# Kernel optimization log

Measured on AMD Instinct MI355X. Metric: run time of the kernel, lower is better.

The kernel has to match this reference:

```python
import jax, jax.numpy as jnp
import numpy as np

N_NODES = 4096
DEG_HALF = 16
MAX_E = 64
D = 128
H = 4
L = 2
N_SPECIES = 4
R_CUT = 5.0
R_TRANS = 3.0


def _layer_norm(x, w, b, eps=1e-5):
    m = jnp.mean(x, axis=-1, keepdims=True)
    v = jnp.mean((x - m) ** 2, axis=-1, keepdims=True)
    return (x - m) * jax.lax.rsqrt(v + eps) * w + b


def _transformer(x, radial_mask, p):
    # x: (N, MAX_E, D); radial_mask: (N, MAX_E). Pre-LN transformer whose
    # attention weights are reweighted by the radial cutoff mask over keys.
    ln1_w, ln1_b, qkv_w, qkv_b, out_w, out_b, ln2_w, ln2_b, m1_w, m1_b, m2_w, m2_b = p
    n, s, d = x.shape
    dh = d // H
    scale = np.float32(1.0 / np.sqrt(dh))
    for l in range(L):
        h = _layer_norm(x, ln1_w[l], ln1_b[l])
        qkv = h @ qkv_w[l] + qkv_b[l]  # (n, s, 3d)
        q, k, v = jnp.split(qkv, 3, axis=-1)
        q = q.reshape(n, s, H, dh).transpose(0, 2, 1, 3)
        k = k.reshape(n, s, H, dh).transpose(0, 2, 1, 3)
        v = v.reshape(n, s, H, dh).transpose(0, 2, 1, 3)
        a = jax.nn.softmax(jnp.einsum("nhqc,nhkc->nhqk", q, k) * scale, axis=-1)
        a = a * radial_mask[:, None, None, :]
        a = a / (jnp.sum(a, axis=-1, keepdims=True) + 1e-9)
        o = jnp.einsum("nhqk,nhkc->nhqc", a, v).transpose(0, 2, 1, 3).reshape(n, s, d)
        x = x + o @ out_w[l] + out_b[l]
        h = _layer_norm(x, ln2_w[l], ln2_b[l])
        x = x + jax.nn.gelu(h @ m1_w[l] + m1_b[l]) @ m2_w[l] + m2_b[l]
    return x


def _forward(edge_vectors, enc_cart_w, enc_center_emb, enc_neighbor_emb, enc_comp_w,
             t0, t1, gnn_w, last_w, comp_w,
             species_index, centers, neighbors, nef_indices, nef_mask,
             nef_to_edges_neighbor, corresponding_edges):
    r = jnp.sqrt(jnp.sum(edge_vectors ** 2, axis=-1))
    radial = jnp.where(r < R_TRANS, 1.0,
                       0.5 * (jnp.cos(jnp.pi * (r - R_TRANS) / (R_CUT - R_TRANS)) + 1.0))
    radial = jnp.where(r < R_CUT, radial, 0.0)
    eic = species_index[centers]
    ein = species_index[neighbors]
    # edge_array_to_nef gathers
    ev_nef = edge_vectors[nef_indices]                  # (N, MAX_E, 3)
    rm = jnp.where(nef_mask, radial[nef_indices], 0.0)  # (N, MAX_E)
    enc = jnp.concatenate([ev_nef @ enc_cart_w,
                           enc_center_emb[eic[nef_indices]],
                           enc_neighbor_emb[ein[nef_indices]]], axis=-1)
    feat = enc @ enc_comp_w                             # (N, MAX_E, D)
    feat = _transformer(feat, rm, t0)
    # one message-passing round (num_gnn_layers=2 -> 1 MP layer)
    edge_feat = feat[centers, nef_to_edges_neighbor]    # NEF -> edge list, (E, D)
    new = jnp.concatenate([edge_feat, edge_feat[corresponding_edges]], axis=-1) @ gnn_w
    new = _transformer(new[nef_indices], rm, t1)        # edge list -> NEF
    feat = feat + new
    node_features = jnp.sum(feat * rm[..., None], axis=1)  # masked scatter-sum
    return node_features @ last_w + comp_w[species_index][:, None]  # (N, 1)


def setup_inputs() -> dict:
    rng = np.random.default_rng(0)
    src = np.repeat(np.arange(N_NODES), DEG_HALF)
    dst = (src + rng.integers(1, N_NODES, size=src.shape[0])) % N_NODES
    centers = np.concatenate([src, dst]).astype(np.int64)
    neighbors = np.concatenate([dst, src]).astype(np.int64)
    E = centers.shape[0]
    corresponding_edges = np.concatenate([np.arange(E // 2, E), np.arange(E // 2)]).astype(np.int64)
    order = np.argsort(centers, kind="stable")
    sc = centers[order]
    starts = np.searchsorted(sc, np.arange(N_NODES))
    ranks = np.arange(E) - starts[sc]
    assert ranks.max() < MAX_E
    nef_indices = np.zeros((N_NODES, MAX_E), np.int64)
    nef_mask = np.zeros((N_NODES, MAX_E), bool)
    nef_indices[sc, ranks] = order
    nef_mask[sc, ranks] = True
    nef_to_edges_neighbor = np.zeros(E, np.int64)
    nef_to_edges_neighbor[order] = ranks
    half = rng.standard_normal((E // 2, 3)) * 1.6
    edge_vectors = np.concatenate([half, -half]).astype(np.float32)
    species_index = rng.integers(0, N_SPECIES, N_NODES).astype(np.int64)

    keys = iter(jax.random.split(jax.random.key(0), 80))

    def lin(shape, fan_in):
        return jax.random.normal(next(keys), shape, jnp.float32) / np.float32(np.sqrt(fan_in))

    inp = {
        "edge_vectors": jnp.asarray(edge_vectors),
        "enc_cart_w": lin((3, D), 3),
        "enc_center_emb": lin((N_SPECIES, D), 1),
        "enc_neighbor_emb": lin((N_SPECIES, D), 1),
        "enc_comp_w": lin((3 * D, D), 3 * D),
        "gnn_w": lin((2 * D, D), 2 * D),
        "last_w": lin((D, 1), D),
        "comp_w": lin((N_SPECIES,), 1),
        "species_index": jnp.asarray(species_index),
        "centers": jnp.asarray(centers),
        "neighbors": jnp.asarray(neighbors),
        "nef_indices": jnp.asarray(nef_indices),
        "nef_mask": jnp.asarray(nef_mask),
        "nef_to_edges_neighbor": jnp.asarray(nef_to_edges_neighbor),
        "corresponding_edges": jnp.asarray(corresponding_edges),
    }
    for t in ("t0", "t1"):
        inp[t + "_ln1_w"] = jnp.ones((L, D), jnp.float32)
        inp[t + "_ln1_b"] = jnp.zeros((L, D), jnp.float32)
        inp[t + "_qkv_w"] = lin((L, D, 3 * D), D)
        inp[t + "_qkv_b"] = jnp.zeros((L, 3 * D), jnp.float32)
        inp[t + "_out_w"] = lin((L, D, D), D)
        inp[t + "_out_b"] = jnp.zeros((L, D), jnp.float32)
        inp[t + "_ln2_w"] = jnp.ones((L, D), jnp.float32)
        inp[t + "_ln2_b"] = jnp.zeros((L, D), jnp.float32)
        inp[t + "_mlp1_w"] = lin((L, D, 4 * D), D)
        inp[t + "_mlp1_b"] = jnp.zeros((L, 4 * D), jnp.float32)
        inp[t + "_mlp2_w"] = lin((L, 4 * D, D), 4 * D)
        inp[t + "_mlp2_b"] = jnp.zeros((L, D), jnp.float32)
    return inp


def reference(edge_vectors, enc_cart_w, enc_center_emb, enc_neighbor_emb, enc_comp_w,
              t0_ln1_w, t0_ln1_b, t0_qkv_w, t0_qkv_b, t0_out_w, t0_out_b,
              t0_ln2_w, t0_ln2_b, t0_mlp1_w, t0_mlp1_b, t0_mlp2_w, t0_mlp2_b,
              t1_ln1_w, t1_ln1_b, t1_qkv_w, t1_qkv_b, t1_out_w, t1_out_b,
              t1_ln2_w, t1_ln2_b, t1_mlp1_w, t1_mlp1_b, t1_mlp2_w, t1_mlp2_b,
              gnn_w, last_w, comp_w,
              species_index, centers, neighbors, nef_indices, nef_mask,
              nef_to_edges_neighbor, corresponding_edges):
    t0 = (t0_ln1_w, t0_ln1_b, t0_qkv_w, t0_qkv_b, t0_out_w, t0_out_b,
          t0_ln2_w, t0_ln2_b, t0_mlp1_w, t0_mlp1_b, t0_mlp2_w, t0_mlp2_b)
    t1 = (t1_ln1_w, t1_ln1_b, t1_qkv_w, t1_qkv_b, t1_out_w, t1_out_b,
          t1_ln2_w, t1_ln2_b, t1_mlp1_w, t1_mlp1_b, t1_mlp2_w, t1_mlp2_b)
    return _forward(edge_vectors, enc_cart_w, enc_center_emb, enc_neighbor_emb, enc_comp_w,
                    t0, t1, gnn_w, last_w, comp_w,
                    species_index, centers, neighbors, nef_indices, nef_mask,
                    nef_to_edges_neighbor, corresponding_edges)
```

## Files before the change

### kernel.cpp

```cpp
#include <hip/hip_runtime.h>

typedef short s8v __attribute__((ext_vector_type(8)));
typedef float f4v __attribute__((ext_vector_type(4)));

#define MFMA16(a,b,c) __builtin_amdgcn_mfma_f32_16x16x32_bf16((a),(b),(c),0,0,0)

#define N_NODES 4096
#define N_EDGE  131072
#define ATT_SCALE 0.17677669529663687f
#define NGC2     -1.5957691216057308f

__device__ __forceinline__ unsigned short f2bf(float f) {
  union { float f; unsigned u; } v; v.f = f;
  return (unsigned short)((v.u + 0x8000u) >> 16);
}
__device__ __forceinline__ unsigned short f2bf_rne(float f) {
  union { float f; unsigned u; } v; v.f = f;
  unsigned r = v.u + 0x7fffu + ((v.u >> 16) & 1u);
  return (unsigned short)(r >> 16);
}
__device__ __forceinline__ float bf2f(short s) {
  union { unsigned u; float f; } v;
  v.u = ((unsigned)(unsigned short)s) << 16;
  return v.f;
}
__device__ __forceinline__ int iclamp(int v, int lo, int hi) {
  return v < lo ? lo : (v > hi ? hi : v);
}


__global__ void k_tr(const float* __restrict__ src, short* __restrict__ dst,
                     int L, int K, int N) {
  int idx = blockIdx.x * 256 + threadIdx.x;
  int tot = L * K * N;
  if (idx >= tot) return;
  int l = idx / (K * N);
  int r = idx - l * (K * N);
  int k = r / N;
  int n = r - k * N;
  dst[l * K * N + n * K + k] = (short)f2bf_rne(src[idx]);
}

__global__ void k_tabs(const float* __restrict__ cart, const float* __restrict__ cemb,
                       const float* __restrict__ nemb, const float* __restrict__ comp,
                       float* __restrict__ tabs) {
  int idx = blockIdx.x * 256 + threadIdx.x;
  if (idx >= 1408) return;
  float s = 0.f;
  if (idx < 384) {
    int i = idx >> 7, d = idx & 127;
    for (int j = 0; j < 128; ++j) s += cart[i * 128 + j] * comp[j * 128 + d];
  } else if (idx < 896) {
    int i2 = idx - 384; int sp = i2 >> 7, d = i2 & 127;
    for (int j = 0; j < 128; ++j) s += cemb[sp * 128 + j] * comp[(128 + j) * 128 + d];
  } else {
    int i2 = idx - 896; int sp = i2 >> 7, d = i2 & 127;
    for (int j = 0; j < 128; ++j) s += nemb[sp * 128 + j] * comp[(256 + j) * 128 + d];
  }
  tabs[idx] = s;
}

__global__ void k_rm(const float* __restrict__ ev, const int* __restrict__ centers,
                     const int* __restrict__ nef2, float* __restrict__ rm) {
  int e = blockIdx.x * 256 + threadIdx.x;
  if (e >= N_EDGE) return;
  float x = ev[e*3], y = ev[e*3+1], z = ev[e*3+2];
  float r = sqrtf(x*x + y*y + z*z);
  float rad;
  if (r < 3.0f)      rad = 1.0f;
  else if (r < 5.0f) rad = 0.5f * (cosf(3.14159265358979f * (r - 3.0f) * 0.5f) + 1.0f);
  else               rad = 0.0f;
  int c  = iclamp(centers[e], 0, N_NODES - 1);
  int rk = iclamp(nef2[e], 0, 63);
  rm[c * 64 + rk] = rad;
}

__global__ __launch_bounds__(256) void k_enc(
    const float* __restrict__ ev, const int* __restrict__ nef,
    const int* __restrict__ centers, const int* __restrict__ neighbors,
    const int* __restrict__ species, const float* __restrict__ tabs,
    short* __restrict__ feat) {
  int n = blockIdx.x, t = threadIdx.x, j = t >> 2, qq = t & 3;
  int e = iclamp(nef[n * 64 + j], 0, N_EDGE - 1);
  float e0 = ev[e*3], e1 = ev[e*3+1], e2 = ev[e*3+2];
  int nc = iclamp(centers[e],   0, N_NODES - 1);
  int nn = iclamp(neighbors[e], 0, N_NODES - 1);
  int sc = iclamp(species[nc], 0, 3), sn = iclamp(species[nn], 0, 3);
  const float* m0 = tabs + qq*32;
  const float* m1 = tabs + 128 + qq*32;
  const float* m2 = tabs + 256 + qq*32;
  const float* tc = tabs + 384 + sc*128 + qq*32;
  const float* tn = tabs + 896 + sn*128 + qq*32;
  short* o = feat + ((size_t)(n*64 + j))*128 + qq*32;
  #pragma unroll
  for (int i = 0; i < 32; i += 2) {
    float a = e0*m0[i]   + e1*m1[i]   + e2*m2[i]   + tc[i]   + tn[i];
    float b = e0*m0[i+1] + e1*m1[i+1] + e2*m2[i+1] + tc[i+1] + tn[i+1];
    *(unsigned*)(o + i) = (unsigned)f2bf_rne(a) | ((unsigned)f2bf_rne(b) << 16);
  }
}


__device__ __forceinline__ void ln_sub(float (&xr)[4][2][4],
                                       const float* __restrict__ gw, const float* __restrict__ gb,
                                       float* red, short* hb, int wid, int quad, int l4) {
  #pragma unroll
  for (int mt = 0; mt < 4; ++mt)
    #pragma unroll
    for (int reg = 0; reg < 4; ++reg) {
      float a = xr[mt][0][reg] + xr[mt][1][reg];
      float s = xr[mt][0][reg]*xr[mt][0][reg] + xr[mt][1][reg]*xr[mt][1][reg];
      #pragma unroll
      for (int m = 1; m < 16; m <<= 1) { a += __shfl_xor(a, m); s += __shfl_xor(s, m); }
      if (l4 == 0) {
        int r = mt*16 + quad*4 + reg;
        red[(wid*64 + r)*2]     = a;
        red[(wid*64 + r)*2 + 1] = s;
      }
    }
  __syncthreads();
  int tid = threadIdx.x;
  if (tid < 64) {
    float a = 0.f, s = 0.f;
    #pragma unroll
    for (int w = 0; w < 4; ++w) { a += red[(w*64 + tid)*2]; s += red[(w*64 + tid)*2 + 1]; }
    float mean = a * (1.f/128.f);
    float var  = s * (1.f/128.f) - mean*mean;
    red[tid*2]     = mean;
    red[tid*2 + 1] = rsqrtf(var + 1e-5f);
  }
  __syncthreads();
  float gv[2], bv[2];
  #pragma unroll
  for (int nt = 0; nt < 2; ++nt) { int c = wid*32 + nt*16 + l4; gv[nt] = gw[c]; bv[nt] = gb[c]; }
  #pragma unroll
  for (int mt = 0; mt < 4; ++mt)
    #pragma unroll
    for (int reg = 0; reg < 4; ++reg) {
      int r = mt*16 + quad*4 + reg;
      float mean = red[r*2], inv = red[r*2 + 1];
      #pragma unroll
      for (int nt = 0; nt < 2; ++nt) {
        float h = (xr[mt][nt][reg] - mean) * inv * gv[nt] + bv[nt];
        hb[r*136 + wid*32 + nt*16 + l4] = (short)f2bf(h);
      }
    }
  __syncthreads();
}

__global__ __launch_bounds__(256, 2) void k_tf(
    short* __restrict__ x, const float* __restrict__ rm,
    const float* __restrict__ lnw1, const float* __restrict__ lnb1,
    const short* __restrict__ qkvT, const float* __restrict__ qkvb,
    const short* __restrict__ outT, const float* __restrict__ outb,
    const float* __restrict__ lnw2, const float* __restrict__ lnb2,
    const short* __restrict__ m1T, const float* __restrict__ m1b,
    const short* __restrict__ m2T, const float* __restrict__ m2b) {
  __shared__ __align__(16) char smem[53248];
  short* hb  = (short*)smem;
  short* kb  = (short*)(smem + 17408);
  short* vtb = (short*)(smem + 34816);
  float* red = (float*)(smem + 34816);

  const int tid = threadIdx.x;
  const int wid = tid >> 6;
  const int lane = tid & 63;
  const int l4 = lane & 15;
  const int quad = lane >> 4;
  const int n = blockIdx.x;

  short* xg = x + (size_t)n * 64 * 128;
  float xr[4][2][4];
  #pragma unroll
  for (int mt = 0; mt < 4; ++mt)
    #pragma unroll
    for (int nt = 0; nt < 2; ++nt)
      #pragma unroll
      for (int reg = 0; reg < 4; ++reg)
        xr[mt][nt][reg] = bf2f(xg[(mt*16 + quad*4 + reg)*128 + wid*32 + nt*16 + l4]);

  for (int l = 0; l < 2; ++l) {
    const float* g1    = lnw1 + l*128;   const float* bb1   = lnb1 + l*128;
    const short* qkvTl = qkvT + l*49152; const float* qkvbl = qkvb + l*384;
    const short* outTl = outT + l*16384; const float* outbl = outb + l*128;
    const float* g2    = lnw2 + l*128;   const float* bb2   = lnb2 + l*128;
    const short* m1Tl  = m1T + l*65536;  const float* m1bl  = m1b + l*512;
    const short* m2Tl  = m2T + l*65536;  const float* m2bl  = m2b + l*128;

    __syncthreads();

    ln_sub(xr, g1, bb1, red, hb, wid, quad, l4);

    #pragma unroll 1
    for (int hh = 0; hh < 2; ++hh) {
      s8v af[2][4];
      #pragma unroll
      for (int m2 = 0; m2 < 2; ++m2)
        #pragma unroll
        for (int k0 = 0; k0 < 4; ++k0)
          af[m2][k0] = *(const s8v*)(hb + ((hh*2 + m2)*16 + l4)*136 + k0*32 + quad*8);
      __syncthreads();

      #pragma unroll 1
      for (int j = 0; j < 6; ++j) {
        int col = wid*96 + j*16 + l4;
        s8v bf[4];
        #pragma unroll
        for (int k0 = 0; k0 < 4; ++k0)
          bf[k0] = *(const s8v*)(qkvTl + col*128 + k0*32 + quad*8);
        float bias = qkvbl[col];
        f4v acc[2];
        #pragma unroll
        for (int m2 = 0; m2 < 2; ++m2) { f4v bb = {bias,bias,bias,bias}; acc[m2] = bb; }
        #pragma unroll
        for (int k0 = 0; k0 < 4; ++k0)
          #pragma unroll
          for (int m2 = 0; m2 < 2; ++m2)
            acc[m2] = MFMA16(af[m2][k0], bf[k0], acc[m2]);
        if (col < 128) {
          #pragma unroll
          for (int m2 = 0; m2 < 2; ++m2)
            #pragma unroll
            for (int reg = 0; reg < 4; ++reg)
              hb[((hh*2+m2)*16 + quad*4 + reg)*136 + col] = (short)f2bf(acc[m2][reg] * ATT_SCALE);
        } else if (col < 256) {
          int c = col - 128;
          #pragma unroll
          for (int m2 = 0; m2 < 2; ++m2)
            #pragma unroll
            for (int reg = 0; reg < 4; ++reg)
              kb[((hh*2+m2)*16 + quad*4 + reg)*136 + c] = (short)f2bf(acc[m2][reg]);
        } else {
          int c = col - 256;
          #pragma unroll
          for (int m2 = 0; m2 < 2; ++m2)
            #pragma unroll
            for (int reg = 0; reg < 4; ++reg)
              vtb[c*72 + (hh*2+m2)*16 + quad*4 + reg] = (short)f2bf(acc[m2][reg]);
        }
      }
    }
    __syncthreads();

    {
      const int h = wid;
      float rv[4];
      #pragma unroll
      for (int n2 = 0; n2 < 4; ++n2) rv[n2] = rm[n*64 + n2*16 + l4];

      #pragma unroll 1
      for (int hh = 0; hh < 2; ++hh) {
        #pragma unroll 1
        for (int m2 = 0; m2 < 2; ++m2) {
          const int row0 = (hh*2 + m2)*16;
          f4v S[4];
          {
            s8v aq = *(const s8v*)(hb + (row0 + l4)*136 + h*32 + quad*8);
            s8v bk0 = *(const s8v*)(kb + (      l4)*136 + h*32 + quad*8);
            s8v bk1 = *(const s8v*)(kb + (16 + l4)*136 + h*32 + quad*8);
            s8v bk2 = *(const s8v*)(kb + (32 + l4)*136 + h*32 + quad*8);
            s8v bk3 = *(const s8v*)(kb + (48 + l4)*136 + h*32 + quad*8);
            f4v zz = {0.f,0.f,0.f,0.f};
            S[0] = MFMA16(aq, bk0, zz);
            S[1] = MFMA16(aq, bk1, zz);
            S[2] = MFMA16(aq, bk2, zz);
            S[3] = MFMA16(aq, bk3, zz);
          }

          #pragma unroll
          for (int reg = 0; reg < 4; ++reg) {
            float mx = fmaxf(fmaxf(S[0][reg], S[1][reg]),
                             fmaxf(S[2][reg], S[3][reg]));
            mx = fmaxf(mx, __shfl_xor(mx, 1));
            mx = fmaxf(mx, __shfl_xor(mx, 2));
            mx = fmaxf(mx, __shfl_xor(mx, 4));
            mx = fmaxf(mx, __shfl_xor(mx, 8));
            float E = 0.f, W = 0.f;
            #pragma unroll
            for (int n2 = 0; n2 < 4; ++n2) {
              float e = __expf(S[n2][reg] - mx);
              E += e; W += e * rv[n2];
              S[n2][reg] = e * rv[n2];
            }
            E += __shfl_xor(E, 1); E += __shfl_xor(E, 2);
            E += __shfl_xor(E, 4); E += __shfl_xor(E, 8);
            W += __shfl_xor(W, 1); W += __shfl_xor(W, 2);
            W += __shfl_xor(W, 4); W += __shfl_xor(W, 8);
            float inv = __builtin_amdgcn_rcpf(W + 1e-9f * E);
            #pragma unroll
            for (int n2 = 0; n2 < 4; ++n2) S[n2][reg] *= inv;
          }

          f4v o[2];
          { f4v zz = {0.f,0.f,0.f,0.f}; o[0] = zz; o[1] = zz; }
          #pragma unroll
          for (int c = 0; c < 2; ++c) {
            #pragma unroll
            for (int n2 = 0; n2 < 2; ++n2)
              #pragma unroll
              for (int reg = 0; reg < 4; ++reg)
                hb[(row0 + quad*4 + reg)*136 + h*32 + n2*16 + l4] =
                    (short)f2bf(S[2*c + n2][reg]);
            s8v ap = *(const s8v*)(hb + (row0 + l4)*136 + h*32 + quad*8);
            #pragma unroll
            for (int nt = 0; nt < 2; ++nt) {
              s8v bv = *(const s8v*)(vtb + (h*32 + nt*16 + l4)*72 + c*32 + quad*8);
              o[nt] = MFMA16(ap, bv, o[nt]);
            }
          }
          #pragma unroll
          for (int nt = 0; nt < 2; ++nt)
            #pragma unroll
            for (int reg = 0; reg < 4; ++reg)
              hb[(row0 + quad*4 + reg)*136 + h*32 + nt*16 + l4] =
                  (short)f2bf(o[nt][reg]);
        }
      }
    }
    __syncthreads();

    #pragma unroll
    for (int hh = 0; hh < 2; ++hh) {
      s8v ao[2][4];
      #pragma unroll
      for (int m2 = 0; m2 < 2; ++m2)
        #pragma unroll
        for (int k0 = 0; k0 < 4; ++k0)
          ao[m2][k0] = *(const s8v*)(hb + ((hh*2+m2)*16 + l4)*136 + k0*32 + quad*8);
      #pragma unroll
      for (int nt = 0; nt < 2; ++nt) {
        int c = wid*32 + nt*16 + l4;
        s8v bo[4];
        #pragma unroll
        for (int k0 = 0; k0 < 4; ++k0)
          bo[k0] = *(const s8v*)(outTl + c*128 + k0*32 + quad*8);
        float bias = outbl[c];
        #pragma unroll
        for (int m2 = 0; m2 < 2; ++m2) {
          int mt = hh*2 + m2;
          f4v a2 = {xr[mt][nt][0] + bias, xr[mt][nt][1] + bias,
                    xr[mt][nt][2] + bias, xr[mt][nt][3] + bias};
          #pragma unroll
          for (int k0 = 0; k0 < 4; ++k0)
            a2 = MFMA16(ao[m2][k0], bo[k0], a2);
          #pragma unroll
          for (int reg = 0; reg < 4; ++reg)
            xr[mt][nt][reg] = a2[reg];
        }
      }
    }

    ln_sub(xr, g2, bb2, red, hb, wid, quad, l4);

    #pragma unroll 1
    for (int cc = 0; cc < 4; ++cc) {
      short* G = (cc & 1) ? vtb : kb;
      #pragma unroll 1
      for (int hh = 0; hh < 2; ++hh) {
        s8v afm[2][4];
        #pragma unroll
        for (int m2 = 0; m2 < 2; ++m2)
          #pragma unroll
          for (int k0 = 0; k0 < 4; ++k0)
            afm[m2][k0] = *(const s8v*)(hb + ((hh*2+m2)*16 + l4)*136 + k0*32 + quad*8);
        #pragma unroll
        for (int nt = 0; nt < 2; ++nt) {
          int jc = cc*128 + wid*32 + nt*16 + l4;
          s8v bm[4];
          #pragma unroll
          for (int k0 = 0; k0 < 4; ++k0)
            bm[k0] = *(const s8v*)(m1Tl + jc*128 + k0*32 + quad*8);
          float bias = m1bl[jc];
          #pragma unroll
          for (int m2 = 0; m2 < 2; ++m2) {
            f4v a2 = {bias, bias, bias, bias};
            #pragma unroll
            for (int k0 = 0; k0 < 4; ++k0)
              a2 = MFMA16(afm[m2][k0], bm[k0], a2);
            #pragma unroll
            for (int reg = 0; reg < 4; ++reg) {
              float v = a2[reg];
              float t = v * v;
              float u = fmaf(0.044715f, t, 1.0f);
              float w = v * u;
              float e = __expf(NGC2 * w);
              float gl = v * __builtin_amdgcn_rcpf(e + 1.0f);
              G[((hh*2+m2)*16 + quad*4 + reg)*136 + wid*32 + nt*16 + l4] = (short)f2bf(gl);
            }
          }
        }
      }
      __syncthreads();
      #pragma unroll
      for (int hh = 0; hh < 2; ++hh) {
        s8v at4[2][4];
        #pragma unroll
        for (int m2 = 0; m2 < 2; ++m2)
          #pragma unroll
          for (int k0 = 0; k0 < 4; ++k0)
            at4[m2][k0] = *(const s8v*)(G + ((hh*2+m2)*16 + l4)*136 + k0*32 + quad*8);
        #pragma unroll
        for (int nt = 0; nt < 2; ++nt) {
          int c = wid*32 + nt*16 + l4;
          s8v b2f[4];
          #pragma unroll
          for (int k0 = 0; k0 < 4; ++k0)
            b2f[k0] = *(const s8v*)(m2Tl + c*512 + cc*128 + k0*32 + quad*8);
          #pragma unroll
          for (int m2 = 0; m2 < 2; ++m2) {
            int mt = hh*2 + m2;
            f4v a2 = {xr[mt][nt][0], xr[mt][nt][1], xr[mt][nt][2], xr[mt][nt][3]};
            #pragma unroll
            for (int k0 = 0; k0 < 4; ++k0)
              a2 = MFMA16(at4[m2][k0], b2f[k0], a2);
            #pragma unroll
            for (int reg = 0; reg < 4; ++reg)
              xr[mt][nt][reg] = a2[reg];
          }
        }
      }
    }
    #pragma unroll
    for (int nt = 0; nt < 2; ++nt) {
      float b = m2bl[wid*32 + nt*16 + l4];
      #pragma unroll
      for (int mt = 0; mt < 4; ++mt)
        #pragma unroll
        for (int reg = 0; reg < 4; ++reg)
          xr[mt][nt][reg] += b;
    }
  }

  #pragma unroll
  for (int mt = 0; mt < 4; ++mt)
    #pragma unroll
    for (int nt = 0; nt < 2; ++nt)
      #pragma unroll
      for (int reg = 0; reg < 4; ++reg)
        xg[(mt*16 + quad*4 + reg)*128 + wid*32 + nt*16 + l4] = (short)f2bf(xr[mt][nt][reg]);
}

__global__ __launch_bounds__(256) void k_gnn(
    const short* __restrict__ feat, const int* __restrict__ nef,
    const int* __restrict__ corr, const int* __restrict__ centers,
    const int* __restrict__ nef2, const short* __restrict__ gnnT,
    short* __restrict__ out) {
  __shared__ __align__(16) short Ab[64 * 264];
  int n = blockIdx.x, t = threadIdx.x;
  int wid = t >> 6, lane = t & 63, l4 = lane & 15, quad = lane >> 4;
  int j = t >> 2, qq = t & 3;
  int e  = iclamp(nef[n*64 + j], 0, N_EDGE - 1);
  int ce = iclamp(corr[e], 0, N_EDGE - 1);
  size_t r1 = ((size_t)iclamp(centers[e],  0, N_NODES-1) * 64 + iclamp(nef2[e],  0, 63)) * 128;
  size_t r2 = ((size_t)iclamp(centers[ce], 0, N_NODES-1) * 64 + iclamp(nef2[ce], 0, 63)) * 128;
  {
    const s8v* p1 = (const s8v*)(feat + r1 + qq*32);
    const s8v* p2 = (const s8v*)(feat + r2 + qq*32);
    #pragma unroll
    for (int ii = 0; ii < 4; ++ii) {
      *(s8v*)(Ab + j*264 + qq*32 + ii*8)       = p1[ii];
      *(s8v*)(Ab + j*264 + 128 + qq*32 + ii*8) = p2[ii];
    }
  }
  __syncthreads();
  f4v acc[4][2];
  #pragma unroll
  for (int mt = 0; mt < 4; ++mt)
    #pragma unroll
    for (int nt = 0; nt < 2; ++nt) { f4v zz = {0.f,0.f,0.f,0.f}; acc[mt][nt] = zz; }
  #pragma unroll
  for (int k0 = 0; k0 < 8; ++k0) {
    s8v a[4];
    #pragma unroll
    for (int mt = 0; mt < 4; ++mt)
      a[mt] = *(const s8v*)(Ab + (mt*16 + l4)*264 + k0*32 + quad*8);
    #pragma unroll
    for (int nt = 0; nt < 2; ++nt) {
      s8v b = *(const s8v*)(gnnT + (wid*32 + nt*16 + l4)*256 + k0*32 + quad*8);
      #pragma unroll
      for (int mt = 0; mt < 4; ++mt)
        acc[mt][nt] = MFMA16(a[mt], b, acc[mt][nt]);
    }
  }
  #pragma unroll
  for (int mt = 0; mt < 4; ++mt)
    #pragma unroll
    for (int nt = 0; nt < 2; ++nt)
      #pragma unroll
      for (int reg = 0; reg < 4; ++reg)
        out[((size_t)n*64 + mt*16 + quad*4 + reg)*128 + wid*32 + nt*16 + l4] =
            (short)f2bf(acc[mt][nt][reg]);
}

__global__ __launch_bounds__(256) void k_final(
    const short* __restrict__ feat, const short* __restrict__ buf2,
    const float* __restrict__ rm, const float* __restrict__ lastw,
    const float* __restrict__ compw, const int* __restrict__ species,
    float* __restrict__ out) {
  __shared__ float part[4];
  int n = blockIdx.x, t = threadIdx.x;
  int wid = t >> 6, lane = t & 63;
  int j = t >> 2, qq = t & 3;
  size_t base = ((size_t)n*64 + j)*128 + qq*32;
  float s = 0.f;
  #pragma unroll
  for (int i = 0; i < 32; ++i)
    s += (bf2f(feat[base + i]) + bf2f(buf2[base + i])) * lastw[qq*32 + i];
  s += __shfl_xor(s, 1);
  s += __shfl_xor(s, 2);
  float v = (qq == 0) ? s * rm[n*64 + j] : 0.f;
  v += __shfl_xor(v, 4);  v += __shfl_xor(v, 8);
  v += __shfl_xor(v, 16); v += __shfl_xor(v, 32);
  if (lane == 0) part[wid] = v;
  __syncthreads();
  if (t == 0) out[n] = part[0] + part[1] + part[2] + part[3]
                       + compw[iclamp(species[n], 0, 3)];
}


extern "C" void kernel_launch(void* const* d_in, const int* in_sizes, int n_in,
                              void* d_out, int out_size, void* d_ws, size_t ws_size,
                              hipStream_t stream) {
  const float* ev      = (const float*)d_in[0];
  const float* cart    = (const float*)d_in[1];
  const float* cemb    = (const float*)d_in[2];
  const float* nemb    = (const float*)d_in[3];
  const float* comp    = (const float*)d_in[4];
  const float* gnnw    = (const float*)d_in[5];
  const float* lastw   = (const float*)d_in[6];
  const float* compw   = (const float*)d_in[7];
  const int*   species = (const int*)d_in[8];
  const int*   centers = (const int*)d_in[9];
  const int*   neighbors = (const int*)d_in[10];
  const int*   nef     = (const int*)d_in[11];
  const int*   nef2    = (const int*)d_in[13];
  const int*   corr    = (const int*)d_in[14];

  const size_t OFF_RM   = 0;
  const size_t OFF_FEAT = 1048576;
  const size_t OFF_BUF2 = 68157440;
  const size_t OFF_TABS = 135266304;
  const size_t OFF_WBF  = 135271936;
  const size_t NEED     = 136910336;
  if (ws_size < NEED) return;

  char* ws = (char*)d_ws;
  float* rm   = (float*)(ws + OFF_RM);
  short* feat = (short*)(ws + OFF_FEAT);
  short* buf2 = (short*)(ws + OFF_BUF2);
  float* tabs = (float*)(ws + OFF_TABS);
  short* wbf  = (short*)(ws + OFF_WBF);

  short* t0q  = wbf + 0;
  short* t0o  = wbf + 98304;
  short* t0m1 = wbf + 131072;
  short* t0m2 = wbf + 262144;
  short* t1q  = wbf + 393216;
  short* t1o  = wbf + 491520;
  short* t1m1 = wbf + 524288;
  short* t1m2 = wbf + 655360;
  short* gnnT = wbf + 786432;

  hipMemsetAsync(rm, 0, 4096*64*sizeof(float), stream);

  k_tr<<<384, 256, 0, stream>>>((const float*)d_in[17], t0q,  2, 128, 384);
  k_tr<<<128, 256, 0, stream>>>((const float*)d_in[19], t0o,  2, 128, 128);
  k_tr<<<512, 256, 0, stream>>>((const float*)d_in[23], t0m1, 2, 128, 512);
  k_tr<<<512, 256, 0, stream>>>((const float*)d_in[25], t0m2, 2, 512, 128);
  k_tr<<<384, 256, 0, stream>>>((const float*)d_in[29], t1q,  2, 128, 384);
  k_tr<<<128, 256, 0, stream>>>((const float*)d_in[31], t1o,  2, 128, 128);
  k_tr<<<512, 256, 0, stream>>>((const float*)d_in[35], t1m1, 2, 128, 512);
  k_tr<<<512, 256, 0, stream>>>((const float*)d_in[37], t1m2, 2, 512, 128);
  k_tr<<<128, 256, 0, stream>>>(gnnw, gnnT, 1, 256, 128);
  k_tabs<<<6, 256, 0, stream>>>(cart, cemb, nemb, comp, tabs);
  k_rm<<<512, 256, 0, stream>>>(ev, centers, nef2, rm);
  k_enc<<<4096, 256, 0, stream>>>(ev, nef, centers, neighbors, species, tabs, feat);

  k_tf<<<4096, 256, 0, stream>>>(feat, rm,
      (const float*)d_in[15], (const float*)d_in[16], t0q, (const float*)d_in[18],
      t0o, (const float*)d_in[20], (const float*)d_in[21], (const float*)d_in[22],
      t0m1, (const float*)d_in[24], t0m2, (const float*)d_in[26]);

  k_gnn<<<4096, 256, 0, stream>>>(feat, nef, corr, centers, nef2, gnnT, buf2);

  k_tf<<<4096, 256, 0, stream>>>(buf2, rm,
      (const float*)d_in[27], (const float*)d_in[28], t1q, (const float*)d_in[30],
      t1o, (const float*)d_in[32], (const float*)d_in[33], (const float*)d_in[34],
      t1m1, (const float*)d_in[36], t1m2, (const float*)d_in[38]);

  k_final<<<4096, 256, 0, stream>>>(feat, buf2, rm, lastw, compw, species, (float*)d_out);
}
```

Baseline: 1.654 ms.

## Split transformer block work across eight waves per node instead of four

```diff
diff --git a/kernel.cpp b/kernel.cpp
--- a/kernel.cpp
+++ b/kernel.cpp
@@ -101,15 +101,15 @@
 }
 
 
-__device__ __forceinline__ void ln_sub(float (&xr)[4][2][4],
-                                       const float* __restrict__ gw, const float* __restrict__ gb,
-                                       float* red, short* hb, int wid, int quad, int l4) {
+__device__ __forceinline__ void ln_sub8(float (&xr)[4][4],
+                                        const float* __restrict__ gw, const float* __restrict__ gb,
+                                        float* red, short* hb, int wid, int quad, int l4, int tid) {
   #pragma unroll
   for (int mt = 0; mt < 4; ++mt)
     #pragma unroll
     for (int reg = 0; reg < 4; ++reg) {
-      float a = xr[mt][0][reg] + xr[mt][1][reg];
-      float s = xr[mt][0][reg]*xr[mt][0][reg] + xr[mt][1][reg]*xr[mt][1][reg];
+      float a = xr[mt][reg];
+      float s = a * a;
       #pragma unroll
       for (int m = 1; m < 16; m <<= 1) { a += __shfl_xor(a, m); s += __shfl_xor(s, m); }
       if (l4 == 0) {
@@ -119,36 +119,31 @@
       }
     }
   __syncthreads();
-  int tid = threadIdx.x;
   if (tid < 64) {
     float a = 0.f, s = 0.f;
     #pragma unroll
-    for (int w = 0; w < 4; ++w) { a += red[(w*64 + tid)*2]; s += red[(w*64 + tid)*2 + 1]; }
+    for (int w = 0; w < 8; ++w) { a += red[(w*64 + tid)*2]; s += red[(w*64 + tid)*2 + 1]; }
     float mean = a * (1.f/128.f);
     float var  = s * (1.f/128.f) - mean*mean;
     red[tid*2]     = mean;
     red[tid*2 + 1] = rsqrtf(var + 1e-5f);
   }
   __syncthreads();
-  float gv[2], bv[2];
-  #pragma unroll
-  for (int nt = 0; nt < 2; ++nt) { int c = wid*32 + nt*16 + l4; gv[nt] = gw[c]; bv[nt] = gb[c]; }
+  int cw = wid*16 + l4;
+  float gv = gw[cw], bvv = gb[cw];
   #pragma unroll
   for (int mt = 0; mt < 4; ++mt)
     #pragma unroll
     for (int reg = 0; reg < 4; ++reg) {
       int r = mt*16 + quad*4 + reg;
       float mean = red[r*2], inv = red[r*2 + 1];
-      #pragma unroll
-      for (int nt = 0; nt < 2; ++nt) {
-        float h = (xr[mt][nt][reg] - mean) * inv * gv[nt] + bv[nt];
-        hb[r*136 + wid*32 + nt*16 + l4] = (short)f2bf(h);
-      }
+      float h = (xr[mt][reg] - mean) * inv * gv + bvv;
+      hb[r*136 + cw] = (short)f2bf(h);
     }
   __syncthreads();
 }
 
-__global__ __launch_bounds__(256, 2) void k_tf(
+__global__ __launch_bounds__(512, 4) void k_tf(
     short* __restrict__ x, const float* __restrict__ rm,
     const float* __restrict__ lnw1, const float* __restrict__ lnb1,
     const short* __restrict__ qkvT, const float* __restrict__ qkvb,
@@ -168,16 +163,15 @@
   const int l4 = lane & 15;
   const int quad = lane >> 4;
   const int n = blockIdx.x;
+  const int cw = wid*16 + l4;
 
   short* xg = x + (size_t)n * 64 * 128;
-  float xr[4][2][4];
+  float xr[4][4];
   #pragma unroll
   for (int mt = 0; mt < 4; ++mt)
     #pragma unroll
-    for (int nt = 0; nt < 2; ++nt)
-      #pragma unroll
-      for (int reg = 0; reg < 4; ++reg)
-        xr[mt][nt][reg] = bf2f(xg[(mt*16 + quad*4 + reg)*128 + wid*32 + nt*16 + l4]);
+    for (int reg = 0; reg < 4; ++reg)
+      xr[mt][reg] = bf2f(xg[(mt*16 + quad*4 + reg)*128 + cw]);
 
   for (int l = 0; l < 2; ++l) {
     const float* g1    = lnw1 + l*128;   const float* bb1   = lnb1 + l*128;
@@ -189,7 +183,7 @@
 
     __syncthreads();
 
-    ln_sub(xr, g1, bb1, red, hb, wid, quad, l4);
+    ln_sub8(xr, g1, bb1, red, hb, wid, quad, l4, tid);
 
     #pragma unroll 1
     for (int hh = 0; hh < 2; ++hh) {
@@ -202,8 +196,8 @@
       __syncthreads();
 
       #pragma unroll 1
-      for (int j = 0; j < 6; ++j) {
-        int col = wid*96 + j*16 + l4;
+      for (int j = 0; j < 3; ++j) {
+        int col = wid*48 + j*16 + l4;
         s8v bf[4];
         #pragma unroll
         for (int k0 = 0; k0 < 4; ++k0)
@@ -243,134 +237,129 @@
     __syncthreads();
 
     {
-      const int h = wid;
+      const int h  = wid >> 1;
+      const int hq = wid & 1;
       float rv[4];
       #pragma unroll
       for (int n2 = 0; n2 < 4; ++n2) rv[n2] = rm[n*64 + n2*16 + l4];
 
       #pragma unroll 1
+      for (int m2 = 0; m2 < 2; ++m2) {
+        const int row0 = hq*32 + m2*16;
+        f4v S[4];
+        {
+          s8v aq = *(const s8v*)(hb + (row0 + l4)*136 + h*32 + quad*8);
+          s8v bk0 = *(const s8v*)(kb + (      l4)*136 + h*32 + quad*8);
+          s8v bk1 = *(const s8v*)(kb + (16 + l4)*136 + h*32 + quad*8);
+          s8v bk2 = *(const s8v*)(kb + (32 + l4)*136 + h*32 + quad*8);
+          s8v bk3 = *(const s8v*)(kb + (48 + l4)*136 + h*32 + quad*8);
+          f4v zz = {0.f,0.f,0.f,0.f};
+          S[0] = MFMA16(aq, bk0, zz);
+          S[1] = MFMA16(aq, bk1, zz);
+          S[2] = MFMA16(aq, bk2, zz);
+          S[3] = MFMA16(aq, bk3, zz);
+        }
+
+        #pragma unroll
+        for (int reg = 0; reg < 4; ++reg) {
+          float mx = fmaxf(fmaxf(S[0][reg], S[1][reg]),
+                           fmaxf(S[2][reg], S[3][reg]));
+          mx = fmaxf(mx, __shfl_xor(mx, 1));
+          mx = fmaxf(mx, __shfl_xor(mx, 2));
+          mx = fmaxf(mx, __shfl_xor(mx, 4));
+          mx = fmaxf(mx, __shfl_xor(mx, 8));
+          float E = 0.f, W = 0.f;
+          #pragma unroll
+          for (int n2 = 0; n2 < 4; ++n2) {
+            float e = __expf(S[n2][reg] - mx);
+            E += e; W += e * rv[n2];
+            S[n2][reg] = e * rv[n2];
+          }
+          E += __shfl_xor(E, 1); E += __shfl_xor(E, 2);
+          E += __shfl_xor(E, 4); E += __shfl_xor(E, 8);
+          W += __shfl_xor(W, 1); W += __shfl_xor(W, 2);
+          W += __shfl_xor(W, 4); W += __shfl_xor(W, 8);
+          float inv = __builtin_amdgcn_rcpf(W + 1e-9f * E);
+          #pragma unroll
+          for (int n2 = 0; n2 < 4; ++n2) S[n2][reg] *= inv;
+        }
+
+        f4v o[2];
+        { f4v zz = {0.f,0.f,0.f,0.f}; o[0] = zz; o[1] = zz; }
+        #pragma unroll
+        for (int c = 0; c < 2; ++c) {
+          #pragma unroll
+          for (int n2 = 0; n2 < 2; ++n2)
+            #pragma unroll
+            for (int reg = 0; reg < 4; ++reg)
+              hb[(row0 + quad*4 + reg)*136 + h*32 + n2*16 + l4] =
+                  (short)f2bf(S[2*c + n2][reg]);
+          s8v ap = *(const s8v*)(hb + (row0 + l4)*136 + h*32 + quad*8);
+          #pragma unroll
+          for (int nt = 0; nt < 2; ++nt) {
+            s8v bv = *(const s8v*)(vtb + (h*32 + nt*16 + l4)*72 + c*32 + quad*8);
+            o[nt] = MFMA16(ap, bv, o[nt]);
+          }
+        }
+        #pragma unroll
+        for (int nt = 0; nt < 2; ++nt)
+          #pragma unroll
+          for (int reg = 0; reg < 4; ++reg)
+            hb[(row0 + quad*4 + reg)*136 + h*32 + nt*16 + l4] =
+                (short)f2bf(o[nt][reg]);
+      }
+    }
+    __syncthreads();
+
+    {
+      s8v bo[4];
+      #pragma unroll
+      for (int k0 = 0; k0 < 4; ++k0)
+        bo[k0] = *(const s8v*)(outTl + cw*128 + k0*32 + quad*8);
+      float bias = outbl[cw];
+      #pragma unroll
       for (int hh = 0; hh < 2; ++hh) {
-        #pragma unroll 1
-        for (int m2 = 0; m2 < 2; ++m2) {
-          const int row0 = (hh*2 + m2)*16;
-          f4v S[4];
-          {
-            s8v aq = *(const s8v*)(hb + (row0 + l4)*136 + h*32 + quad*8);
-            s8v bk0 = *(const s8v*)(kb + (      l4)*136 + h*32 + quad*8);
-            s8v bk1 = *(const s8v*)(kb + (16 + l4)*136 + h*32 + quad*8);
-            s8v bk2 = *(const s8v*)(kb + (32 + l4)*136 + h*32 + quad*8);
-            s8v bk3 = *(const s8v*)(kb + (48 + l4)*136 + h*32 + quad*8);
-            f4v zz = {0.f,0.f,0.f,0.f};
-            S[0] = MFMA16(aq, bk0, zz);
-            S[1] = MFMA16(aq, bk1, zz);
-            S[2] = MFMA16(aq, bk2, zz);
-            S[3] = MFMA16(aq, bk3, zz);
-          }
-
-          #pragma unroll
-          for (int reg = 0; reg < 4; ++reg) {
-            float mx = fmaxf(fmaxf(S[0][reg], S[1][reg]),
-                             fmaxf(S[2][reg], S[3][reg]));
-            mx = fmaxf(mx, __shfl_xor(mx, 1));
-            mx = fmaxf(mx, __shfl_xor(mx, 2));
-            mx = fmaxf(mx, __shfl_xor(mx, 4));
-            mx = fmaxf(mx, __shfl_xor(mx, 8));
-            float E = 0.f, W = 0.f;
-            #pragma unroll
-            for (int n2 = 0; n2 < 4; ++n2) {
-              float e = __expf(S[n2][reg] - mx);
-              E += e; W += e * rv[n2];
-              S[n2][reg] = e * rv[n2];
-            }
-            E += __shfl_xor(E, 1); E += __shfl_xor(E, 2);
-            E += __shfl_xor(E, 4); E += __shfl_xor(E, 8);
-            W += __shfl_xor(W, 1); W += __shfl_xor(W, 2);
-            W += __shfl_xor(W, 4); W += __shfl_xor(W, 8);
-            float inv = __builtin_amdgcn_rcpf(W + 1e-9f * E);
-            #pragma unroll
-            for (int n2 = 0; n2 < 4; ++n2) S[n2][reg] *= inv;
-          }
-
-          f4v o[2];
-          { f4v zz = {0.f,0.f,0.f,0.f}; o[0] = zz; o[1] = zz; }
-          #pragma unroll
-          for (int c = 0; c < 2; ++c) {
-            #pragma unroll
-            for (int n2 = 0; n2 < 2; ++n2)
-              #pragma unroll
-              for (int reg = 0; reg < 4; ++reg)
-                hb[(row0 + quad*4 + reg)*136 + h*32 + n2*16 + l4] =
-                    (short)f2bf(S[2*c + n2][reg]);
-            s8v ap = *(const s8v*)(hb + (row0 + l4)*136 + h*32 + quad*8);
-            #pragma unroll
-            for (int nt = 0; nt < 2; ++nt) {
-              s8v bv = *(const s8v*)(vtb + (h*32 + nt*16 + l4)*72 + c*32 + quad*8);
-              o[nt] = MFMA16(ap, bv, o[nt]);
-            }
-          }
-          #pragma unroll
-          for (int nt = 0; nt < 2; ++nt)
-            #pragma unroll
-            for (int reg = 0; reg < 4; ++reg)
-              hb[(row0 + quad*4 + reg)*136 + h*32 + nt*16 + l4] =
-                  (short)f2bf(o[nt][reg]);
-        }
-      }
-    }
-    __syncthreads();
-
-    #pragma unroll
-    for (int hh = 0; hh < 2; ++hh) {
-      s8v ao[2][4];
-      #pragma unroll
-      for (int m2 = 0; m2 < 2; ++m2)
-        #pragma unroll
-        for (int k0 = 0; k0 < 4; ++k0)
-          ao[m2][k0] = *(const s8v*)(hb + ((hh*2+m2)*16 + l4)*136 + k0*32 + quad*8);
-      #pragma unroll
-      for (int nt = 0; nt < 2; ++nt) {
-        int c = wid*32 + nt*16 + l4;
-        s8v bo[4];
-        #pragma unroll
-        for (int k0 = 0; k0 < 4; ++k0)
-          bo[k0] = *(const s8v*)(outTl + c*128 + k0*32 + quad*8);
-        float bias = outbl[c];
+        s8v ao[2][4];
+        #pragma unroll
+        for (int m2 = 0; m2 < 2; ++m2)
+          #pragma unroll
+          for (int k0 = 0; k0 < 4; ++k0)
+            ao[m2][k0] = *(const s8v*)(hb + ((hh*2+m2)*16 + l4)*136 + k0*32 + quad*8);
         #pragma unroll
         for (int m2 = 0; m2 < 2; ++m2) {
           int mt = hh*2 + m2;
-          f4v a2 = {xr[mt][nt][0] + bias, xr[mt][nt][1] + bias,
-                    xr[mt][nt][2] + bias, xr[mt][nt][3] + bias};
+          f4v a2 = {xr[mt][0] + bias, xr[mt][1] + bias,
+                    xr[mt][2] + bias, xr[mt][3] + bias};
           #pragma unroll
           for (int k0 = 0; k0 < 4; ++k0)
             a2 = MFMA16(ao[m2][k0], bo[k0], a2);
           #pragma unroll
           for (int reg = 0; reg < 4; ++reg)
-            xr[mt][nt][reg] = a2[reg];
+            xr[mt][reg] = a2[reg];
         }
       }
     }
 
-    ln_sub(xr, g2, bb2, red, hb, wid, quad, l4);
+    ln_sub8(xr, g2, bb2, red, hb, wid, quad, l4, tid);
 
     #pragma unroll 1
     for (int cc = 0; cc < 4; ++cc) {
       short* G = (cc & 1) ? vtb : kb;
-      #pragma unroll 1
-      for (int hh = 0; hh < 2; ++hh) {
-        s8v afm[2][4];
-        #pragma unroll
-        for (int m2 = 0; m2 < 2; ++m2)
-          #pragma unroll
-          for (int k0 = 0; k0 < 4; ++k0)
-            afm[m2][k0] = *(const s8v*)(hb + ((hh*2+m2)*16 + l4)*136 + k0*32 + quad*8);
-        #pragma unroll
-        for (int nt = 0; nt < 2; ++nt) {
-          int jc = cc*128 + wid*32 + nt*16 + l4;
-          s8v bm[4];
-          #pragma unroll
-          for (int k0 = 0; k0 < 4; ++k0)
-            bm[k0] = *(const s8v*)(m1Tl + jc*128 + k0*32 + quad*8);
-          float bias = m1bl[jc];
+      {
+        int jc = cc*128 + cw;
+        s8v bm[4];
+        #pragma unroll
+        for (int k0 = 0; k0 < 4; ++k0)
+          bm[k0] = *(const s8v*)(m1Tl + jc*128 + k0*32 + quad*8);
+        float bias = m1bl[jc];
+        #pragma unroll 1
+        for (int hh = 0; hh < 2; ++hh) {
+          s8v afm[2][4];
+          #pragma unroll
+          for (int m2 = 0; m2 < 2; ++m2)
+            #pragma unroll
+            for (int k0 = 0; k0 < 4; ++k0)
+              afm[m2][k0] = *(const s8v*)(hb + ((hh*2+m2)*16 + l4)*136 + k0*32 + quad*8);
           #pragma unroll
           for (int m2 = 0; m2 < 2; ++m2) {
             f4v a2 = {bias, bias, bias, bias};
@@ -385,59 +374,54 @@
               float w = v * u;
               float e = __expf(NGC2 * w);
               float gl = v * __builtin_amdgcn_rcpf(e + 1.0f);
-              G[((hh*2+m2)*16 + quad*4 + reg)*136 + wid*32 + nt*16 + l4] = (short)f2bf(gl);
+              G[((hh*2+m2)*16 + quad*4 + reg)*136 + cw] = (short)f2bf(gl);
             }
           }
         }
       }
       __syncthreads();
-      #pragma unroll
-      for (int hh = 0; hh < 2; ++hh) {
-        s8v at4[2][4];
-        #pragma unroll
-        for (int m2 = 0; m2 < 2; ++m2)
-          #pragma unroll
-          for (int k0 = 0; k0 < 4; ++k0)
-            at4[m2][k0] = *(const s8v*)(G + ((hh*2+m2)*16 + l4)*136 + k0*32 + quad*8);
-        #pragma unroll
-        for (int nt = 0; nt < 2; ++nt) {
-          int c = wid*32 + nt*16 + l4;
-          s8v b2f[4];
-          #pragma unroll
-          for (int k0 = 0; k0 < 4; ++k0)
-            b2f[k0] = *(const s8v*)(m2Tl + c*512 + cc*128 + k0*32 + quad*8);
+      {
+        s8v b2f[4];
+        #pragma unroll
+        for (int k0 = 0; k0 < 4; ++k0)
+          b2f[k0] = *(const s8v*)(m2Tl + cw*512 + cc*128 + k0*32 + quad*8);
+        #pragma unroll
+        for (int hh = 0; hh < 2; ++hh) {
+          s8v at4[2][4];
+          #pragma unroll
+          for (int m2 = 0; m2 < 2; ++m2)
+            #pragma unroll
+            for (int k0 = 0; k0 < 4; ++k0)
+              at4[m2][k0] = *(const s8v*)(G + ((hh*2+m2)*16 + l4)*136 + k0*32 + quad*8);
           #pragma unroll
           for (int m2 = 0; m2 < 2; ++m2) {
             int mt = hh*2 + m2;
-            f4v a2 = {xr[mt][nt][0], xr[mt][nt][1], xr[mt][nt][2], xr[mt][nt][3]};
+            f4v a2 = {xr[mt][0], xr[mt][1], xr[mt][2], xr[mt][3]};
             #pragma unroll
             for (int k0 = 0; k0 < 4; ++k0)
               a2 = MFMA16(at4[m2][k0], b2f[k0], a2);
             #pragma unroll
             for (int reg = 0; reg < 4; ++reg)
-              xr[mt][nt][reg] = a2[reg];
+              xr[mt][reg] = a2[reg];
           }
         }
       }
     }
-    #pragma unroll
-    for (int nt = 0; nt < 2; ++nt) {
-      float b = m2bl[wid*32 + nt*16 + l4];
+    {
+      float b = m2bl[cw];
       #pragma unroll
       for (int mt = 0; mt < 4; ++mt)
         #pragma unroll
         for (int reg = 0; reg < 4; ++reg)
-          xr[mt][nt][reg] += b;
+          xr[mt][reg] += b;
     }
   }
 
   #pragma unroll
   for (int mt = 0; mt < 4; ++mt)
     #pragma unroll
-    for (int nt = 0; nt < 2; ++nt)
-      #pragma unroll
-      for (int reg = 0; reg < 4; ++reg)
-        xg[(mt*16 + quad*4 + reg)*128 + wid*32 + nt*16 + l4] = (short)f2bf(xr[mt][nt][reg]);
+    for (int reg = 0; reg < 4; ++reg)
+      xg[(mt*16 + quad*4 + reg)*128 + cw] = (short)f2bf(xr[mt][reg]);
 }
 
 __global__ __launch_bounds__(256) void k_gnn(
@@ -576,14 +560,14 @@
   k_rm<<<512, 256, 0, stream>>>(ev, centers, nef2, rm);
   k_enc<<<4096, 256, 0, stream>>>(ev, nef, centers, neighbors, species, tabs, feat);
 
-  k_tf<<<4096, 256, 0, stream>>>(feat, rm,
+  k_tf<<<4096, 512, 0, stream>>>(feat, rm,
       (const float*)d_in[15], (const float*)d_in[16], t0q, (const float*)d_in[18],
       t0o, (const float*)d_in[20], (const float*)d_in[21], (const float*)d_in[22],
       t0m1, (const float*)d_in[24], t0m2, (const float*)d_in[26]);
 
   k_gnn<<<4096, 256, 0, stream>>>(feat, nef, corr, centers, nef2, gnnT, buf2);
 
-  k_tf<<<4096, 256, 0, stream>>>(buf2, rm,
+  k_tf<<<4096, 512, 0, stream>>>(buf2, rm,
       (const float*)d_in[27], (const float*)d_in[28], t1q, (const float*)d_in[30],
       t1o, (const float*)d_in[32], (const float*)d_in[33], (const float*)d_in[34],
       t1m1, (const float*)d_in[36], t1m2, (const float*)d_in[38]);
```

Result: slower. 1.815 ms (+9.7%).
